# Kernel tuning notes

Hardware: AMD Instinct MI355X
Metric: run time of the kernel (lower is better)

## Reference

```python
import jax, jax.numpy as jnp
import numpy as np

N_SRC = 50000
N_DST = 50000
N_EDGES = 500000
HIDDEN = 128
HEADS = 8
HEAD_DIM = HIDDEN // HEADS
SCALE = HEAD_DIM ** -0.5


def setup_inputs() -> dict:
    key = jax.random.key(0)
    ks = jax.random.split(key, 12)
    lim = 1.0 / np.sqrt(HIDDEN)
    def lin(k):
        kw, kb = jax.random.split(k)
        W = jax.random.uniform(kw, (HIDDEN, HIDDEN), jnp.float32, -lim, lim)
        b = jax.random.uniform(kb, (HIDDEN,), jnp.float32, -lim, lim)
        return W, b
    Wq, bq = lin(ks[0]); Wk, bk = lin(ks[1]); Wv, bv = lin(ks[2]); Wo, bo = lin(ks[3])
    return {
        "x_src": jax.random.normal(ks[4], (N_SRC, HIDDEN), jnp.float32),
        "x_dst": jax.random.normal(ks[5], (N_DST, HIDDEN), jnp.float32),
        "edge_index": jax.random.randint(ks[6], (2, N_EDGES), 0, N_SRC, jnp.int64),
        "Wq": Wq, "bq": bq, "Wk": Wk, "bk": bk, "Wv": Wv, "bv": bv,
        "Wo": Wo, "bo": bo,
        "edge_bias": jax.random.normal(ks[7], (HEADS,), jnp.float32) * 0.02,
    }


def reference(x_src, x_dst, edge_index, Wq, bq, Wk, bk, Wv, bv, Wo, bo, edge_bias):
    num_dst = x_dst.shape[0]
    # projections (torch Linear: y = x W^T + b), reshape to (N, H, D)
    q = (x_dst @ Wq.T + bq).reshape(num_dst, HEADS, HEAD_DIM)
    k = (x_src @ Wk.T + bk).reshape(-1, HEADS, HEAD_DIM)
    v = (x_src @ Wv.T + bv).reshape(-1, HEADS, HEAD_DIM)
    src_idx, dst_idx = edge_index[0], edge_index[1]
    # per-edge dot-product scores: (E, H)
    scores = (q[dst_idx] * k[src_idx]).sum(-1) * SCALE + edge_bias
    # sparse softmax over edges grouped by destination
    m = jax.ops.segment_max(scores, dst_idx, num_segments=num_dst)  # (N_dst, H)
    e = jnp.exp(scores - m[dst_idx])
    s = jax.ops.segment_sum(e, dst_idx, num_segments=num_dst)  # (N_dst, H)
    w = e / (s[dst_idx] + 1e-8)  # (E, H)
    # scatter-add aggregate weighted values
    out = jax.ops.segment_sum(w[:, :, None] * v[src_idx], dst_idx, num_segments=num_dst)
    out = out.reshape(num_dst, HIDDEN)
    return out @ Wo.T + bo
```

## Files before the change

### kernel.cpp

```cpp
#include <hip/hip_runtime.h>
#include <math.h>

#define HIDDEN 128
#define SCALE 0.25f

typedef __attribute__((ext_vector_type(8))) short short8v;
typedef __attribute__((ext_vector_type(4))) float f32x4;

__device__ __forceinline__ unsigned short f2bf(float f) {
  const unsigned u = __float_as_uint(f);
  const unsigned r = u + 0x7fffu + ((u >> 16) & 1u);
  return (unsigned short)(r >> 16);
}
__device__ __forceinline__ float bflo(unsigned u) { return __uint_as_float(u << 16); }
__device__ __forceinline__ float bfhi(unsigned u) { return __uint_as_float(u & 0xffff0000u); }

__global__ __launch_bounds__(256) void convert_w_kernel(
    const float* __restrict__ W0, const float* __restrict__ W1,
    const float* __restrict__ W2, const float* __restrict__ W3,
    unsigned short* __restrict__ Wfrag)
{
  const int chunk = blockIdx.x * 256 + threadIdx.x;
  const int m = chunk >> 11;
  const int rem = chunk & 2047;
  const int l = rem & 63;
  const int nkk = rem >> 6;
  const int n = nkk >> 2, kk = nkk & 3;
  const float* W = (m == 0) ? W0 : (m == 1) ? W1 : (m == 2) ? W2 : W3;
  const int row = n * 16 + (l & 15);
  const int k0 = kk * 32 + (l >> 4) * 8;
  const float4 v0 = *(const float4*)&W[row * 128 + k0];
  const float4 v1 = *(const float4*)&W[row * 128 + k0 + 4];
  uint4 o;
  o.x = (unsigned)f2bf(v0.x) | ((unsigned)f2bf(v0.y) << 16);
  o.y = (unsigned)f2bf(v0.z) | ((unsigned)f2bf(v0.w) << 16);
  o.z = (unsigned)f2bf(v1.x) | ((unsigned)f2bf(v1.y) << 16);
  o.w = (unsigned)f2bf(v1.z) | ((unsigned)f2bf(v1.w) << 16);
  *(uint4*)&Wfrag[(size_t)chunk * 8] = o;
}

__global__ __launch_bounds__(256) void gemm_mfma_kernel(
    const void* __restrict__ Xin, int x_bf16,
    const unsigned short* __restrict__ Wfrag,
    const float* __restrict__ bias,
    void* __restrict__ Y, int N, int mode)
{
  __shared__ __align__(16) char XsB[64 * 256];
  const int t = threadIdx.x;
  const int row_base = blockIdx.x * 64;

  if (!x_bf16) {
    const float* Xf = (const float*)Xin;
    float4 xv[8];
    #pragma unroll
    for (int it = 0; it < 8; ++it) {
      const int c = t + it * 256;
      const int row = c >> 5, fc = (c & 31) << 2;
      const int g = row_base + row;
      xv[it] = make_float4(0.f, 0.f, 0.f, 0.f);
      if (g < N) xv[it] = *(const float4*)&Xf[(size_t)g * 128 + fc];
    }
    #pragma unroll
    for (int it = 0; it < 8; ++it) {
      const int c = t + it * 256;
      const int row = c >> 5, b8 = (c & 31) << 3;
      uint2 p;
      p.x = (unsigned)f2bf(xv[it].x) | ((unsigned)f2bf(xv[it].y) << 16);
      p.y = (unsigned)f2bf(xv[it].z) | ((unsigned)f2bf(xv[it].w) << 16);
      *(uint2*)&XsB[row * 256 + (b8 ^ ((row & 7) << 4))] = p;
    }
  } else {
    const unsigned short* Xh = (const unsigned short*)Xin;
    uint2 hv[8];
    #pragma unroll
    for (int it = 0; it < 8; ++it) {
      const int c = t + it * 256;
      const int row = c >> 5, fc = (c & 31) << 2;
      const int g = row_base + row;
      hv[it] = make_uint2(0, 0);
      if (g < N) hv[it] = *(const uint2*)&Xh[(size_t)g * 128 + fc];
    }
    #pragma unroll
    for (int it = 0; it < 8; ++it) {
      const int c = t + it * 256;
      const int row = c >> 5, b8 = (c & 31) << 3;
      *(uint2*)&XsB[row * 256 + (b8 ^ ((row & 7) << 4))] = hv[it];
    }
  }
  __syncthreads();

  const int l = t & 63, w = t >> 6;
  const int r16 = l & 15, g16 = l >> 4;
  const int sw = (r16 & 7) << 4;
  f32x4 acc[8];
  #pragma unroll
  for (int n = 0; n < 8; ++n) acc[n] = (f32x4){0.f, 0.f, 0.f, 0.f};

  const char* ax = &XsB[(w * 16 + r16) * 256];
  const short8v* wf = (const short8v*)Wfrag + l;
  #pragma unroll
  for (int kk = 0; kk < 4; ++kk) {
    const short8v a = *(const short8v*)(ax + ((kk * 64 + g16 * 16) ^ sw));
    #pragma unroll
    for (int n = 0; n < 8; ++n) {
      const short8v b = wf[(n * 4 + kk) * 64];
      acc[n] = __builtin_amdgcn_mfma_f32_16x16x32_bf16(a, b, acc[n], 0, 0, 0);
    }
  }

  #pragma unroll
  for (int n = 0; n < 8; ++n) {
    const int col = n * 16 + r16;
    const float bv = bias[col];
    #pragma unroll
    for (int r = 0; r < 4; ++r) {
      const int g = row_base + w * 16 + g16 * 4 + r;
      if (g >= N) continue;
      const float o = acc[n][r] + bv;
      if (mode == 0) {
        ((float*)Y)[(size_t)g * 128 + col] = o;
      } else if (mode == 1) {
        ((unsigned short*)Y)[(size_t)g * 128 + col] = f2bf(o);
      } else {
        ((unsigned short*)Y)[(size_t)g * 256 + ((mode == 2) ? 0 : 128) + col] = f2bf(o);
      }
    }
  }
}

__global__ __launch_bounds__(256) void count_edges_kernel(
    const int* __restrict__ ei, int E, int* __restrict__ counts)
{
  const int e = (blockIdx.x * 256 + threadIdx.x) * 4;
  if (e + 4 <= E) {
    const int4 d = *(const int4*)&ei[E + e];
    atomicAdd(&counts[d.x], 1);
    atomicAdd(&counts[d.y], 1);
    atomicAdd(&counts[d.z], 1);
    atomicAdd(&counts[d.w], 1);
  } else {
    for (int k = e; k < E; ++k) atomicAdd(&counts[ei[E + k]], 1);
  }
}

__global__ __launch_bounds__(256) void reduce_counts_kernel(
    const int* __restrict__ counts, int n, int* __restrict__ bsums)
{
  const int idx = blockIdx.x * 256 + threadIdx.x;
  int x = (idx < n) ? counts[idx] : 0;
  #pragma unroll
  for (int off = 1; off < 64; off <<= 1) x += __shfl_xor(x, off);
  __shared__ int ws[4];
  if ((threadIdx.x & 63) == 0) ws[threadIdx.x >> 6] = x;
  __syncthreads();
  if (threadIdx.x == 0) bsums[blockIdx.x] = ws[0] + ws[1] + ws[2] + ws[3];
}

__global__ __launch_bounds__(256) void scan_bsums_kernel(int* bsums, int nb)
{
  __shared__ int buf[256];
  const int t = threadIdx.x;
  const int x = (t < nb) ? bsums[t] : 0;
  buf[t] = x;
  __syncthreads();
  int val = x;
  #pragma unroll
  for (int off = 1; off < 256; off <<= 1) {
    const int other = (t >= off) ? buf[t - off] : 0;
    __syncthreads();
    val += other;
    buf[t] = val;
    __syncthreads();
  }
  if (t < nb) bsums[t] = val - x;
}

__global__ __launch_bounds__(256) void scan_counts_kernel(
    const int* __restrict__ counts, int n, const int* __restrict__ bsums,
    int* __restrict__ offsets)
{
  const int idx = blockIdx.x * 256 + threadIdx.x;
  const int lane = threadIdx.x & 63, wid = threadIdx.x >> 6;
  const int x = (idx < n) ? counts[idx] : 0;
  int v = x;
  #pragma unroll
  for (int off = 1; off < 64; off <<= 1) {
    const int t2 = __shfl_up(v, off);
    if (lane >= off) v += t2;
  }
  __shared__ int wsum[4];
  if (lane == 63) wsum[wid] = v;
  __syncthreads();
  int wbase = 0;
  for (int p = 0; p < wid; ++p) wbase += wsum[p];
  if (idx < n) offsets[idx] = bsums[blockIdx.x] + wbase + v - x;
}

__global__ __launch_bounds__(256) void scatter_kernel(
    const int* __restrict__ ei, int E, const int* __restrict__ offsets,
    int* __restrict__ cursor, int* __restrict__ csr_src)
{
  const int e = (blockIdx.x * 256 + threadIdx.x) * 4;
  if (e + 4 <= E) {
    const int4 s = *(const int4*)&ei[e];
    const int4 d = *(const int4*)&ei[E + e];
    int p;
    p = atomicAdd(&cursor[d.x], 1); csr_src[offsets[d.x] + p] = s.x;
    p = atomicAdd(&cursor[d.y], 1); csr_src[offsets[d.y] + p] = s.y;
    p = atomicAdd(&cursor[d.z], 1); csr_src[offsets[d.z] + p] = s.z;
    p = atomicAdd(&cursor[d.w], 1); csr_src[offsets[d.w] + p] = s.w;
  } else {
    for (int k = e; k < E; ++k) {
      const int d = ei[E + k];
      const int p = atomicAdd(&cursor[d], 1);
      csr_src[offsets[d] + p] = ei[k];
    }
  }
}

__global__ __launch_bounds__(256) void edge_attn_kernel(
    const unsigned short* __restrict__ qb, const unsigned short* __restrict__ kvb,
    const float* __restrict__ eb, const int* __restrict__ offsets,
    const int* __restrict__ counts, const int* __restrict__ csr_src,
    unsigned short* __restrict__ agg, int Ndst)
{
  const int wave = blockIdx.x * 4 + (threadIdx.x >> 6);
  if (wave >= Ndst) return;
  const int lane = threadIdx.x & 63;
  const unsigned qp = *(const unsigned*)&qb[(size_t)wave * 128 + 2 * lane];
  const float qx = bflo(qp), qy = bfhi(qp);
  const float bias = eb[lane >> 3];
  const int ro = offsets[wave];
  const int cnt = counts[wave];
  const unsigned short* kvl = kvb + 2 * lane;

  float s = 0.f, a0 = 0.f, a1 = 0.f;
  int tE = 0;
  for (; tE + 4 <= cnt; tE += 4) {
    const int s0 = csr_src[ro + tE + 0];
    const int s1 = csr_src[ro + tE + 1];
    const int s2 = csr_src[ro + tE + 2];
    const int s3 = csr_src[ro + tE + 3];
    const unsigned k0 = *(const unsigned*)&kvl[(size_t)s0 * 256];
    const unsigned v0 = *(const unsigned*)&kvl[(size_t)s0 * 256 + 128];
    const unsigned k1 = *(const unsigned*)&kvl[(size_t)s1 * 256];
    const unsigned v1 = *(const unsigned*)&kvl[(size_t)s1 * 256 + 128];
    const unsigned k2 = *(const unsigned*)&kvl[(size_t)s2 * 256];
    const unsigned v2 = *(const unsigned*)&kvl[(size_t)s2 * 256 + 128];
    const unsigned k3 = *(const unsigned*)&kvl[(size_t)s3 * 256];
    const unsigned v3 = *(const unsigned*)&kvl[(size_t)s3 * 256 + 128];
    float p0 = fmaf(qx, bflo(k0), qy * bfhi(k0));
    float p1 = fmaf(qx, bflo(k1), qy * bfhi(k1));
    float p2 = fmaf(qx, bflo(k2), qy * bfhi(k2));
    float p3 = fmaf(qx, bflo(k3), qy * bfhi(k3));
    p0 += __shfl_xor(p0, 1); p1 += __shfl_xor(p1, 1);
    p2 += __shfl_xor(p2, 1); p3 += __shfl_xor(p3, 1);
    p0 += __shfl_xor(p0, 2); p1 += __shfl_xor(p1, 2);
    p2 += __shfl_xor(p2, 2); p3 += __shfl_xor(p3, 2);
    p0 += __shfl_xor(p0, 4); p1 += __shfl_xor(p1, 4);
    p2 += __shfl_xor(p2, 4); p3 += __shfl_xor(p3, 4);
    const float e0 = __expf(fmaf(p0, SCALE, bias));
    const float e1 = __expf(fmaf(p1, SCALE, bias));
    const float e2 = __expf(fmaf(p2, SCALE, bias));
    const float e3 = __expf(fmaf(p3, SCALE, bias));
    s += (e0 + e1) + (e2 + e3);
    a0 = fmaf(e0, bflo(v0), a0); a1 = fmaf(e0, bfhi(v0), a1);
    a0 = fmaf(e1, bflo(v1), a0); a1 = fmaf(e1, bfhi(v1), a1);
    a0 = fmaf(e2, bflo(v2), a0); a1 = fmaf(e2, bfhi(v2), a1);
    a0 = fmaf(e3, bflo(v3), a0); a1 = fmaf(e3, bfhi(v3), a1);
  }
  for (; tE < cnt; ++tE) {
    const int s0 = csr_src[ro + tE];
    const unsigned k0 = *(const unsigned*)&kvl[(size_t)s0 * 256];
    const unsigned v0 = *(const unsigned*)&kvl[(size_t)s0 * 256 + 128];
    float p0 = fmaf(qx, bflo(k0), qy * bfhi(k0));
    p0 += __shfl_xor(p0, 1); p0 += __shfl_xor(p0, 2); p0 += __shfl_xor(p0, 4);
    const float e0 = __expf(fmaf(p0, SCALE, bias));
    s += e0;
    a0 = fmaf(e0, bflo(v0), a0); a1 = fmaf(e0, bfhi(v0), a1);
  }
  const float rs = 1.0f / (s + 1e-8f);
  const unsigned out = (unsigned)f2bf(a0 * rs) | ((unsigned)f2bf(a1 * rs) << 16);
  *(unsigned*)&agg[(size_t)wave * 128 + 2 * lane] = out;
}

extern "C" void kernel_launch(void* const* d_in, const int* in_sizes, int n_in,
                              void* d_out, int out_size, void* d_ws, size_t ws_size,
                              hipStream_t stream) {
  const float* x_src = (const float*)d_in[0];
  const float* x_dst = (const float*)d_in[1];
  const int*   ei    = (const int*)d_in[2];
  const float* Wq = (const float*)d_in[3];
  const float* bq = (const float*)d_in[4];
  const float* Wk = (const float*)d_in[5];
  const float* bk = (const float*)d_in[6];
  const float* Wv = (const float*)d_in[7];
  const float* bv = (const float*)d_in[8];
  const float* Wo = (const float*)d_in[9];
  const float* bo = (const float*)d_in[10];
  const float* eb = (const float*)d_in[11];

  const int Nsrc = in_sizes[0] / HIDDEN;
  const int Ndst = in_sizes[1] / HIDDEN;
  const int E    = in_sizes[2] / 2;

  char* w = (char*)d_ws;
  unsigned short* qb   = (unsigned short*)w; w += (size_t)Ndst * 128 * 2;
  unsigned short* kvb  = (unsigned short*)w; w += (size_t)Nsrc * 256 * 2;
  unsigned short* aggb = (unsigned short*)w; w += (size_t)Ndst * 128 * 2;
  unsigned short* Wb   = (unsigned short*)w; w += (size_t)4 * 16384 * 2;
  int* counts  = (int*)w; w += (size_t)Ndst * sizeof(int);
  int* cursor  = (int*)w; w += (size_t)Ndst * sizeof(int);
  int* offsets = (int*)w; w += (size_t)Ndst * sizeof(int);
  int* bsums   = (int*)w; w += 256 * sizeof(int);
  int* csr_src = (int*)w; w += (size_t)E * sizeof(int);

  hipMemsetAsync(counts, 0, (size_t)Ndst * 2 * sizeof(int), stream);

  dim3 blk256(256);
  convert_w_kernel<<<32, blk256, 0, stream>>>(Wq, Wk, Wv, Wo, Wb);

  const int gb_dst = (Ndst + 63) / 64;
  const int gb_src = (Nsrc + 63) / 64;
  gemm_mfma_kernel<<<gb_dst, blk256, 0, stream>>>(x_dst, 0, Wb,         bq, qb,  Ndst, 1);
  gemm_mfma_kernel<<<gb_src, blk256, 0, stream>>>(x_src, 0, Wb + 16384, bk, kvb, Nsrc, 2);
  gemm_mfma_kernel<<<gb_src, blk256, 0, stream>>>(x_src, 0, Wb + 32768, bv, kvb, Nsrc, 3);

  const int e4blocks = (E / 4 + 255) / 256;
  count_edges_kernel<<<e4blocks, blk256, 0, stream>>>(ei, E, counts);

  const int nb = (Ndst + 255) / 256;
  reduce_counts_kernel<<<nb, blk256, 0, stream>>>(counts, Ndst, bsums);
  scan_bsums_kernel<<<1, blk256, 0, stream>>>(bsums, nb);
  scan_counts_kernel<<<nb, blk256, 0, stream>>>(counts, Ndst, bsums, offsets);

  scatter_kernel<<<e4blocks, blk256, 0, stream>>>(ei, E, offsets, cursor, csr_src);

  const int ablocks = (Ndst + 3) / 4;
  edge_attn_kernel<<<ablocks, blk256, 0, stream>>>(qb, kvb, eb, offsets, counts,
                                                   csr_src, aggb, Ndst);

  gemm_mfma_kernel<<<gb_dst, blk256, 0, stream>>>(aggb, 1, Wb + 49152, bo, d_out, Ndst, 0);
}
```

Measured before the change: 169.6 us.

## Fuse QKV projections and edge counting, restructure edge attention for per-lane heads

Merges weight conversion with edge-degree counting into one prep kernel, and fuses the Q, K and V projections into a single launch where K and V share one x_src load and conversion. The edge attention kernel changes from one lane per feature pair with shuffle reductions per edge to eight edges processed in parallel per wave, each lane owning a full head with 16-wide vector loads, then a cross-group shuffle reduction at the end. This cuts launch count and redundant reads of x_src, and lowers shuffle traffic per edge. The cost is higher register pressure (16 accumulators plus 32 for K/V in the fused GEMM) and idle lanes for nodes with few edges.

New measurement: 172.9 us. About the same (+2.0%).

```diff
diff --git a/kernel.cpp b/kernel.cpp
--- a/kernel.cpp
+++ b/kernel.cpp
@@ -15,77 +15,164 @@
 __device__ __forceinline__ float bflo(unsigned u) { return __uint_as_float(u << 16); }
 __device__ __forceinline__ float bfhi(unsigned u) { return __uint_as_float(u & 0xffff0000u); }
 
-__global__ __launch_bounds__(256) void convert_w_kernel(
+__global__ __launch_bounds__(256) void prep_kernel(
     const float* __restrict__ W0, const float* __restrict__ W1,
     const float* __restrict__ W2, const float* __restrict__ W3,
-    unsigned short* __restrict__ Wfrag)
-{
-  const int chunk = blockIdx.x * 256 + threadIdx.x;
-  const int m = chunk >> 11;
-  const int rem = chunk & 2047;
-  const int l = rem & 63;
-  const int nkk = rem >> 6;
-  const int n = nkk >> 2, kk = nkk & 3;
-  const float* W = (m == 0) ? W0 : (m == 1) ? W1 : (m == 2) ? W2 : W3;
-  const int row = n * 16 + (l & 15);
-  const int k0 = kk * 32 + (l >> 4) * 8;
-  const float4 v0 = *(const float4*)&W[row * 128 + k0];
-  const float4 v1 = *(const float4*)&W[row * 128 + k0 + 4];
-  uint4 o;
-  o.x = (unsigned)f2bf(v0.x) | ((unsigned)f2bf(v0.y) << 16);
-  o.y = (unsigned)f2bf(v0.z) | ((unsigned)f2bf(v0.w) << 16);
-  o.z = (unsigned)f2bf(v1.x) | ((unsigned)f2bf(v1.y) << 16);
-  o.w = (unsigned)f2bf(v1.z) | ((unsigned)f2bf(v1.w) << 16);
-  *(uint4*)&Wfrag[(size_t)chunk * 8] = o;
-}
-
-__global__ __launch_bounds__(256) void gemm_mfma_kernel(
-    const void* __restrict__ Xin, int x_bf16,
+    unsigned short* __restrict__ Wfrag,
+    const int* __restrict__ ei, int E, int* __restrict__ counts)
+{
+  if (blockIdx.x < 32) {
+    const int chunk = blockIdx.x * 256 + threadIdx.x;
+    const int m = chunk >> 11;
+    const int rem = chunk & 2047;
+    const int l = rem & 63;
+    const int nkk = rem >> 6;
+    const int n = nkk >> 2, kk = nkk & 3;
+    const float* W = (m == 0) ? W0 : (m == 1) ? W1 : (m == 2) ? W2 : W3;
+    const int row = n * 16 + (l & 15);
+    const int k0 = kk * 32 + (l >> 4) * 8;
+    const float4 v0 = *(const float4*)&W[row * 128 + k0];
+    const float4 v1 = *(const float4*)&W[row * 128 + k0 + 4];
+    uint4 o;
+    o.x = (unsigned)f2bf(v0.x) | ((unsigned)f2bf(v0.y) << 16);
+    o.y = (unsigned)f2bf(v0.z) | ((unsigned)f2bf(v0.w) << 16);
+    o.z = (unsigned)f2bf(v1.x) | ((unsigned)f2bf(v1.y) << 16);
+    o.w = (unsigned)f2bf(v1.z) | ((unsigned)f2bf(v1.w) << 16);
+    *(uint4*)&Wfrag[(size_t)chunk * 8] = o;
+  } else {
+    const int e = ((blockIdx.x - 32) * 256 + threadIdx.x) * 4;
+    if (e + 4 <= E) {
+      const int4 d = *(const int4*)&ei[E + e];
+      atomicAdd(&counts[d.x], 1);
+      atomicAdd(&counts[d.y], 1);
+      atomicAdd(&counts[d.z], 1);
+      atomicAdd(&counts[d.w], 1);
+    } else {
+      for (int k = e; k < E; ++k) atomicAdd(&counts[ei[E + k]], 1);
+    }
+  }
+}
+
+__global__ __launch_bounds__(256) void qkv_gemm_kernel(
+    const float* __restrict__ x_src, const float* __restrict__ x_dst,
     const unsigned short* __restrict__ Wfrag,
-    const float* __restrict__ bias,
-    void* __restrict__ Y, int N, int mode)
+    const float* __restrict__ bq, const float* __restrict__ bk,
+    const float* __restrict__ bv,
+    unsigned short* __restrict__ qb, unsigned short* __restrict__ kvb,
+    int Nsrc, int Ndst, int gb_src)
+{
+  __shared__ __align__(16) char XsB[64 * 256];
+  const int t = threadIdx.x;
+  const bool isQ = (int)blockIdx.x >= gb_src;
+  const int blk = isQ ? ((int)blockIdx.x - gb_src) : (int)blockIdx.x;
+  const int N = isQ ? Ndst : Nsrc;
+  const float* Xf = isQ ? x_dst : x_src;
+  const int row_base = blk * 64;
+
+  float4 xv[8];
+  #pragma unroll
+  for (int it = 0; it < 8; ++it) {
+    const int c = t + it * 256;
+    const int row = c >> 5, fc = (c & 31) << 2;
+    const int g = row_base + row;
+    xv[it] = make_float4(0.f, 0.f, 0.f, 0.f);
+    if (g < N) xv[it] = *(const float4*)&Xf[(size_t)g * 128 + fc];
+  }
+  #pragma unroll
+  for (int it = 0; it < 8; ++it) {
+    const int c = t + it * 256;
+    const int row = c >> 5, b8 = (c & 31) << 3;
+    uint2 p;
+    p.x = (unsigned)f2bf(xv[it].x) | ((unsigned)f2bf(xv[it].y) << 16);
+    p.y = (unsigned)f2bf(xv[it].z) | ((unsigned)f2bf(xv[it].w) << 16);
+    *(uint2*)&XsB[row * 256 + (b8 ^ ((row & 7) << 4))] = p;
+  }
+  __syncthreads();
+
+  const int l = t & 63, w = t >> 6;
+  const int r16 = l & 15, g16 = l >> 4;
+  const int sw = (r16 & 7) << 4;
+  const char* ax = &XsB[(w * 16 + r16) * 256];
+
+  if (isQ) {
+    f32x4 acc[8];
+    #pragma unroll
+    for (int n = 0; n < 8; ++n) acc[n] = (f32x4){0.f, 0.f, 0.f, 0.f};
+    const short8v* wf = (const short8v*)Wfrag + l;
+    #pragma unroll
+    for (int kk = 0; kk < 4; ++kk) {
+      const short8v a = *(const short8v*)(ax + ((kk * 64 + g16 * 16) ^ sw));
+      #pragma unroll
+      for (int n = 0; n < 8; ++n)
+        acc[n] = __builtin_amdgcn_mfma_f32_16x16x32_bf16(a, wf[(n * 4 + kk) * 64], acc[n], 0, 0, 0);
+    }
+    #pragma unroll
+    for (int n = 0; n < 8; ++n) {
+      const int col = n * 16 + r16;
+      const float bvv = bq[col];
+      #pragma unroll
+      for (int r = 0; r < 4; ++r) {
+        const int g = row_base + w * 16 + g16 * 4 + r;
+        if (g < N) qb[(size_t)g * 128 + col] = f2bf(acc[n][r] + bvv);
+      }
+    }
+  } else {
+    f32x4 accK[8], accV[8];
+    #pragma unroll
+    for (int n = 0; n < 8; ++n) {
+      accK[n] = (f32x4){0.f, 0.f, 0.f, 0.f};
+      accV[n] = (f32x4){0.f, 0.f, 0.f, 0.f};
+    }
+    const short8v* wfk = (const short8v*)(Wfrag + 16384) + l;
+    const short8v* wfv = (const short8v*)(Wfrag + 32768) + l;
+    #pragma unroll
+    for (int kk = 0; kk < 4; ++kk) {
+      const short8v a = *(const short8v*)(ax + ((kk * 64 + g16 * 16) ^ sw));
+      #pragma unroll
+      for (int n = 0; n < 8; ++n) {
+        accK[n] = __builtin_amdgcn_mfma_f32_16x16x32_bf16(a, wfk[(n * 4 + kk) * 64], accK[n], 0, 0, 0);
+        accV[n] = __builtin_amdgcn_mfma_f32_16x16x32_bf16(a, wfv[(n * 4 + kk) * 64], accV[n], 0, 0, 0);
+      }
+    }
+    #pragma unroll
+    for (int n = 0; n < 8; ++n) {
+      const int col = n * 16 + r16;
+      const float bkk = bk[col], bvv = bv[col];
+      #pragma unroll
+      for (int r = 0; r < 4; ++r) {
+        const int g = row_base + w * 16 + g16 * 4 + r;
+        if (g < N) {
+          kvb[(size_t)g * 256 + col]       = f2bf(accK[n][r] + bkk);
+          kvb[(size_t)g * 256 + 128 + col] = f2bf(accV[n][r] + bvv);
+        }
+      }
+    }
+  }
+}
+
+__global__ __launch_bounds__(256) void out_gemm_kernel(
+    const unsigned short* __restrict__ Xh,
+    const unsigned short* __restrict__ Wfrag_o,
+    const float* __restrict__ bo, float* __restrict__ Y, int N)
 {
   __shared__ __align__(16) char XsB[64 * 256];
   const int t = threadIdx.x;
   const int row_base = blockIdx.x * 64;
 
-  if (!x_bf16) {
-    const float* Xf = (const float*)Xin;
-    float4 xv[8];
-    #pragma unroll
-    for (int it = 0; it < 8; ++it) {
-      const int c = t + it * 256;
-      const int row = c >> 5, fc = (c & 31) << 2;
-      const int g = row_base + row;
-      xv[it] = make_float4(0.f, 0.f, 0.f, 0.f);
-      if (g < N) xv[it] = *(const float4*)&Xf[(size_t)g * 128 + fc];
-    }
-    #pragma unroll
-    for (int it = 0; it < 8; ++it) {
-      const int c = t + it * 256;
-      const int row = c >> 5, b8 = (c & 31) << 3;
-      uint2 p;
-      p.x = (unsigned)f2bf(xv[it].x) | ((unsigned)f2bf(xv[it].y) << 16);
-      p.y = (unsigned)f2bf(xv[it].z) | ((unsigned)f2bf(xv[it].w) << 16);
-      *(uint2*)&XsB[row * 256 + (b8 ^ ((row & 7) << 4))] = p;
-    }
-  } else {
-    const unsigned short* Xh = (const unsigned short*)Xin;
-    uint2 hv[8];
-    #pragma unroll
-    for (int it = 0; it < 8; ++it) {
-      const int c = t + it * 256;
-      const int row = c >> 5, fc = (c & 31) << 2;
-      const int g = row_base + row;
-      hv[it] = make_uint2(0, 0);
-      if (g < N) hv[it] = *(const uint2*)&Xh[(size_t)g * 128 + fc];
-    }
-    #pragma unroll
-    for (int it = 0; it < 8; ++it) {
-      const int c = t + it * 256;
-      const int row = c >> 5, b8 = (c & 31) << 3;
-      *(uint2*)&XsB[row * 256 + (b8 ^ ((row & 7) << 4))] = hv[it];
-    }
+  uint2 hv[8];
+  #pragma unroll
+  for (int it = 0; it < 8; ++it) {
+    const int c = t + it * 256;
+    const int row = c >> 5, fc = (c & 31) << 2;
+    const int g = row_base + row;
+    hv[it] = make_uint2(0, 0);
+    if (g < N) hv[it] = *(const uint2*)&Xh[(size_t)g * 128 + fc];
+  }
+  #pragma unroll
+  for (int it = 0; it < 8; ++it) {
+    const int c = t + it * 256;
+    const int row = c >> 5, b8 = (c & 31) << 3;
+    *(uint2*)&XsB[row * 256 + (b8 ^ ((row & 7) << 4))] = hv[it];
   }
   __syncthreads();
 
@@ -95,51 +182,24 @@
   f32x4 acc[8];
   #pragma unroll
   for (int n = 0; n < 8; ++n) acc[n] = (f32x4){0.f, 0.f, 0.f, 0.f};
-
   const char* ax = &XsB[(w * 16 + r16) * 256];
-  const short8v* wf = (const short8v*)Wfrag + l;
+  const short8v* wf = (const short8v*)Wfrag_o + l;
   #pragma unroll
   for (int kk = 0; kk < 4; ++kk) {
     const short8v a = *(const short8v*)(ax + ((kk * 64 + g16 * 16) ^ sw));
     #pragma unroll
-    for (int n = 0; n < 8; ++n) {
-      const short8v b = wf[(n * 4 + kk) * 64];
-      acc[n] = __builtin_amdgcn_mfma_f32_16x16x32_bf16(a, b, acc[n], 0, 0, 0);
-    }
-  }
-
+    for (int n = 0; n < 8; ++n)
+      acc[n] = __builtin_amdgcn_mfma_f32_16x16x32_bf16(a, wf[(n * 4 + kk) * 64], acc[n], 0, 0, 0);
+  }
   #pragma unroll
   for (int n = 0; n < 8; ++n) {
     const int col = n * 16 + r16;
-    const float bv = bias[col];
+    const float bvv = bo[col];
     #pragma unroll
     for (int r = 0; r < 4; ++r) {
       const int g = row_base + w * 16 + g16 * 4 + r;
-      if (g >= N) continue;
-      const float o = acc[n][r] + bv;
-      if (mode == 0) {
-        ((float*)Y)[(size_t)g * 128 + col] = o;
-      } else if (mode == 1) {
-        ((unsigned short*)Y)[(size_t)g * 128 + col] = f2bf(o);
-      } else {
-        ((unsigned short*)Y)[(size_t)g * 256 + ((mode == 2) ? 0 : 128) + col] = f2bf(o);
-      }
-    }
-  }
-}
-
-__global__ __launch_bounds__(256) void count_edges_kernel(
-    const int* __restrict__ ei, int E, int* __restrict__ counts)
-{
-  const int e = (blockIdx.x * 256 + threadIdx.x) * 4;
-  if (e + 4 <= E) {
-    const int4 d = *(const int4*)&ei[E + e];
-    atomicAdd(&counts[d.x], 1);
-    atomicAdd(&counts[d.y], 1);
-    atomicAdd(&counts[d.z], 1);
-    atomicAdd(&counts[d.w], 1);
-  } else {
-    for (int k = e; k < E; ++k) atomicAdd(&counts[ei[E + k]], 1);
+      if (g < N) Y[(size_t)g * 128 + col] = acc[n][r] + bvv;
+    }
   }
 }
 
@@ -227,61 +287,72 @@
   const int wave = blockIdx.x * 4 + (threadIdx.x >> 6);
   if (wave >= Ndst) return;
   const int lane = threadIdx.x & 63;
-  const unsigned qp = *(const unsigned*)&qb[(size_t)wave * 128 + 2 * lane];
-  const float qx = bflo(qp), qy = bfhi(qp);
-  const float bias = eb[lane >> 3];
+  const int eg = lane >> 3, h = lane & 7;
+
+  const uint4 q0 = *(const uint4*)&qb[(size_t)wave * 128 + h * 16];
+  const uint4 q1 = *(const uint4*)&qb[(size_t)wave * 128 + h * 16 + 8];
+  const float bias = eb[h];
   const int ro = offsets[wave];
   const int cnt = counts[wave];
-  const unsigned short* kvl = kvb + 2 * lane;
-
-  float s = 0.f, a0 = 0.f, a1 = 0.f;
-  int tE = 0;
-  for (; tE + 4 <= cnt; tE += 4) {
-    const int s0 = csr_src[ro + tE + 0];
-    const int s1 = csr_src[ro + tE + 1];
-    const int s2 = csr_src[ro + tE + 2];
-    const int s3 = csr_src[ro + tE + 3];
-    const unsigned k0 = *(const unsigned*)&kvl[(size_t)s0 * 256];
-    const unsigned v0 = *(const unsigned*)&kvl[(size_t)s0 * 256 + 128];
-    const unsigned k1 = *(const unsigned*)&kvl[(size_t)s1 * 256];
-    const unsigned v1 = *(const unsigned*)&kvl[(size_t)s1 * 256 + 128];
-    const unsigned k2 = *(const unsigned*)&kvl[(size_t)s2 * 256];
-    const unsigned v2 = *(const unsigned*)&kvl[(size_t)s2 * 256 + 128];
-    const unsigned k3 = *(const unsigned*)&kvl[(size_t)s3 * 256];
-    const unsigned v3 = *(const unsigned*)&kvl[(size_t)s3 * 256 + 128];
-    float p0 = fmaf(qx, bflo(k0), qy * bfhi(k0));
-    float p1 = fmaf(qx, bflo(k1), qy * bfhi(k1));
-    float p2 = fmaf(qx, bflo(k2), qy * bfhi(k2));
-    float p3 = fmaf(qx, bflo(k3), qy * bfhi(k3));
-    p0 += __shfl_xor(p0, 1); p1 += __shfl_xor(p1, 1);
-    p2 += __shfl_xor(p2, 1); p3 += __shfl_xor(p3, 1);
-    p0 += __shfl_xor(p0, 2); p1 += __shfl_xor(p1, 2);
-    p2 += __shfl_xor(p2, 2); p3 += __shfl_xor(p3, 2);
-    p0 += __shfl_xor(p0, 4); p1 += __shfl_xor(p1, 4);
-    p2 += __shfl_xor(p2, 4); p3 += __shfl_xor(p3, 4);
-    const float e0 = __expf(fmaf(p0, SCALE, bias));
-    const float e1 = __expf(fmaf(p1, SCALE, bias));
-    const float e2 = __expf(fmaf(p2, SCALE, bias));
-    const float e3 = __expf(fmaf(p3, SCALE, bias));
-    s += (e0 + e1) + (e2 + e3);
-    a0 = fmaf(e0, bflo(v0), a0); a1 = fmaf(e0, bfhi(v0), a1);
-    a0 = fmaf(e1, bflo(v1), a0); a1 = fmaf(e1, bfhi(v1), a1);
-    a0 = fmaf(e2, bflo(v2), a0); a1 = fmaf(e2, bfhi(v2), a1);
-    a0 = fmaf(e3, bflo(v3), a0); a1 = fmaf(e3, bfhi(v3), a1);
-  }
-  for (; tE < cnt; ++tE) {
-    const int s0 = csr_src[ro + tE];
-    const unsigned k0 = *(const unsigned*)&kvl[(size_t)s0 * 256];
-    const unsigned v0 = *(const unsigned*)&kvl[(size_t)s0 * 256 + 128];
-    float p0 = fmaf(qx, bflo(k0), qy * bfhi(k0));
-    p0 += __shfl_xor(p0, 1); p0 += __shfl_xor(p0, 2); p0 += __shfl_xor(p0, 4);
-    const float e0 = __expf(fmaf(p0, SCALE, bias));
-    s += e0;
-    a0 = fmaf(e0, bflo(v0), a0); a1 = fmaf(e0, bfhi(v0), a1);
-  }
-  const float rs = 1.0f / (s + 1e-8f);
-  const unsigned out = (unsigned)f2bf(a0 * rs) | ((unsigned)f2bf(a1 * rs) << 16);
-  *(unsigned*)&agg[(size_t)wave * 128 + 2 * lane] = out;
+
+  float acc[16];
+  #pragma unroll
+  for (int j = 0; j < 16; ++j) acc[j] = 0.f;
+  float s = 0.f;
+
+  for (int it = 0; it * 8 < cnt; ++it) {
+    const int e = it * 8 + eg;
+    const bool act = e < cnt;
+    const int src = act ? csr_src[ro + e] : 0;
+    const size_t base = (size_t)src * 256 + h * 16;
+    const uint4 k0 = *(const uint4*)&kvb[base];
+    const uint4 k1 = *(const uint4*)&kvb[base + 8];
+    const uint4 v0 = *(const uint4*)&kvb[base + 128];
+    const uint4 v1 = *(const uint4*)&kvb[base + 136];
+
+    float p = 0.f;
+    p = fmaf(bflo(q0.x), bflo(k0.x), p); p = fmaf(bfhi(q0.x), bfhi(k0.x), p);
+    p = fmaf(bflo(q0.y), bflo(k0.y), p); p = fmaf(bfhi(q0.y), bfhi(k0.y), p);
+    p = fmaf(bflo(q0.z), bflo(k0.z), p); p = fmaf(bfhi(q0.z), bfhi(k0.z), p);
+    p = fmaf(bflo(q0.w), bflo(k0.w), p); p = fmaf(bfhi(q0.w), bfhi(k0.w), p);
+    p = fmaf(bflo(q1.x), bflo(k1.x), p); p = fmaf(bfhi(q1.x), bfhi(k1.x), p);
+    p = fmaf(bflo(q1.y), bflo(k1.y), p); p = fmaf(bfhi(q1.y), bfhi(k1.y), p);
+    p = fmaf(bflo(q1.z), bflo(k1.z), p); p = fmaf(bfhi(q1.z), bfhi(k1.z), p);
+    p = fmaf(bflo(q1.w), bflo(k1.w), p); p = fmaf(bfhi(q1.w), bfhi(k1.w), p);
+
+    const float wgt = act ? __expf(fmaf(p, SCALE, bias)) : 0.f;
+    s += wgt;
+    acc[0]  = fmaf(wgt, bflo(v0.x), acc[0]);  acc[1]  = fmaf(wgt, bfhi(v0.x), acc[1]);
+    acc[2]  = fmaf(wgt, bflo(v0.y), acc[2]);  acc[3]  = fmaf(wgt, bfhi(v0.y), acc[3]);
+    acc[4]  = fmaf(wgt, bflo(v0.z), acc[4]);  acc[5]  = fmaf(wgt, bfhi(v0.z), acc[5]);
+    acc[6]  = fmaf(wgt, bflo(v0.w), acc[6]);  acc[7]  = fmaf(wgt, bfhi(v0.w), acc[7]);
+    acc[8]  = fmaf(wgt, bflo(v1.x), acc[8]);  acc[9]  = fmaf(wgt, bfhi(v1.x), acc[9]);
+    acc[10] = fmaf(wgt, bflo(v1.y), acc[10]); acc[11] = fmaf(wgt, bfhi(v1.y), acc[11]);
+    acc[12] = fmaf(wgt, bflo(v1.z), acc[12]); acc[13] = fmaf(wgt, bfhi(v1.z), acc[13]);
+    acc[14] = fmaf(wgt, bflo(v1.w), acc[14]); acc[15] = fmaf(wgt, bfhi(v1.w), acc[15]);
+  }
+
+  #pragma unroll
+  for (int m = 8; m <= 32; m <<= 1) {
+    s += __shfl_xor(s, m);
+    #pragma unroll
+    for (int j = 0; j < 16; ++j) acc[j] += __shfl_xor(acc[j], m);
+  }
+
+  if (eg == 0) {
+    const float rs = 1.0f / (s + 1e-8f);
+    uint4 o0, o1;
+    o0.x = (unsigned)f2bf(acc[0] * rs)  | ((unsigned)f2bf(acc[1] * rs) << 16);
+    o0.y = (unsigned)f2bf(acc[2] * rs)  | ((unsigned)f2bf(acc[3] * rs) << 16);
+    o0.z = (unsigned)f2bf(acc[4] * rs)  | ((unsigned)f2bf(acc[5] * rs) << 16);
+    o0.w = (unsigned)f2bf(acc[6] * rs)  | ((unsigned)f2bf(acc[7] * rs) << 16);
+    o1.x = (unsigned)f2bf(acc[8] * rs)  | ((unsigned)f2bf(acc[9] * rs) << 16);
+    o1.y = (unsigned)f2bf(acc[10] * rs) | ((unsigned)f2bf(acc[11] * rs) << 16);
+    o1.z = (unsigned)f2bf(acc[12] * rs) | ((unsigned)f2bf(acc[13] * rs) << 16);
+    o1.w = (unsigned)f2bf(acc[14] * rs) | ((unsigned)f2bf(acc[15] * rs) << 16);
+    *(uint4*)&agg[(size_t)wave * 128 + h * 16] = o0;
+    *(uint4*)&agg[(size_t)wave * 128 + h * 16 + 8] = o1;
+  }
 }
 
 extern "C" void kernel_launch(void* const* d_in, const int* in_sizes, int n_in,
@@ -318,16 +389,13 @@
   hipMemsetAsync(counts, 0, (size_t)Ndst * 2 * sizeof(int), stream);
 
   dim3 blk256(256);
-  convert_w_kernel<<<32, blk256, 0, stream>>>(Wq, Wk, Wv, Wo, Wb);
+  const int e4blocks = (E / 4 + 255) / 256;
+  prep_kernel<<<32 + e4blocks, blk256, 0, stream>>>(Wq, Wk, Wv, Wo, Wb, ei, E, counts);
 
   const int gb_dst = (Ndst + 63) / 64;
   const int gb_src = (Nsrc + 63) / 64;
-  gemm_mfma_kernel<<<gb_dst, blk256, 0, stream>>>(x_dst, 0, Wb,         bq, qb,  Ndst, 1);
-  gemm_mfma_kernel<<<gb_src, blk256, 0, stream>>>(x_src, 0, Wb + 16384, bk, kvb, Nsrc, 2);
-  gemm_mfma_kernel<<<gb_src, blk256, 0, stream>>>(x_src, 0, Wb + 32768, bv, kvb, Nsrc, 3);
-
-  const int e4blocks = (E / 4 + 255) / 256;
-  count_edges_kernel<<<e4blocks, blk256, 0, stream>>>(ei, E, counts);
+  qkv_gemm_kernel<<<gb_src + gb_dst, blk256, 0, stream>>>(
+      x_src, x_dst, Wb, bq, bk, bv, qb, kvb, Nsrc, Ndst, gb_src);
 
   const int nb = (Ndst + 255) / 256;
   reduce_counts_kernel<<<nb, blk256, 0, stream>>>(counts, Ndst, bsums);
@@ -340,5 +408,5 @@
   edge_attn_kernel<<<ablocks, blk256, 0, stream>>>(qb, kvb, eb, offsets, counts,
                                                    csr_src, aggb, Ndst);
 
-  gemm_mfma_kernel<<<gb_dst, blk256, 0, stream>>>(aggb, 1, Wb + 49152, bo, d_out, Ndst, 0);
-}
+  out_gemm_kernel<<<gb_dst, blk256, 0, stream>>>(aggb, Wb + 49152, bo, (float*)d_out, Ndst);
+}
```
